# Performance work log

Measured on AMD Instinct MI355X. Metric: run time of the kernel, lower is better.

## Reference

```python
import jax, jax.numpy as jnp
import numpy as np

BN_EPS = 1e-5

# Binary activation with hardtanh STE semantics (forward: sign)
@jax.custom_vjp
def binary_act(x):
    return jnp.sign(x)

def _ba_fwd(x):
    return jnp.sign(x), x

def _ba_bwd(x, g):
    return (jnp.where(jnp.abs(x) > 1.0, 0.0, g),)

binary_act.defvjp(_ba_fwd, _ba_bwd)

# Binary weight quantizer (forward: sign, backward: identity STE)
@jax.custom_vjp
def binary_w(x):
    return jnp.sign(x)

def _bw_fwd(x):
    return jnp.sign(x), None

def _bw_bwd(_, g):
    return (g,)

binary_w.defvjp(_bw_fwd, _bw_bwd)


def setup_inputs() -> dict:
    key = jax.random.key(0)
    k1, k2, k3 = jax.random.split(key, 3)
    B, C_in, H, W_sp = 32, 256, 56, 56
    C_out, KH, KW = 256, 3, 3
    x = jax.random.normal(k1, (B, C_in, H, W_sp), dtype=jnp.float32)
    weight = jax.random.normal(k2, (C_out, C_in, KH, KW), dtype=jnp.float32) * 0.05
    bias = jax.random.normal(k3, (C_out,), dtype=jnp.float32) * 0.01
    gamma = jnp.ones((C_out,), dtype=jnp.float32)
    beta = jnp.zeros((C_out,), dtype=jnp.float32)
    return {"x": x, "weight": weight, "bias": bias, "gamma": gamma, "beta": beta}


def reference(x, weight, bias, gamma, beta):
    # --- activation binarization (A=2): sign ---
    xb = binary_act(x)
    # --- weight binarization (W=2): mean-center over in-channel dim, clamp, sign * alpha ---
    wc = weight - jnp.mean(weight, axis=1, keepdims=True)
    wc = jnp.clip(wc, -1.0, 1.0)
    alpha = jnp.mean(jnp.abs(wc), axis=(1, 2, 3), keepdims=True)  # per-output-channel scale
    wq = binary_w(wc) * alpha
    # --- conv2d, stride 1, padding 1 ---
    y = jax.lax.conv_general_dilated(
        xb, wq, window_strides=(1, 1), padding=((1, 1), (1, 1)),
        dimension_numbers=("NCHW", "OIHW", "NCHW"))
    y = y + bias[None, :, None, None]
    # --- BatchNorm2d (training-mode batch statistics, biased variance) ---
    mu = jnp.mean(y, axis=(0, 2, 3), keepdims=True)
    var = jnp.var(y, axis=(0, 2, 3), keepdims=True)
    y = (y - mu) * jax.lax.rsqrt(var + BN_EPS)
    y = y * gamma[None, :, None, None] + beta[None, :, None, None]
    # --- last_relu=1 ---
    y = jax.nn.relu(y)
    # --- last_bin=1 (A=2 -> binary activation) ---
    y = binary_act(y)
    return y
```

## Files before the change

### kernel.cpp

```cpp
#include <hip/hip_runtime.h>

typedef unsigned long long u64;
typedef int i32x4 __attribute__((ext_vector_type(4)));
typedef int i32x16 __attribute__((ext_vector_type(16)));

#define N_SP 3136
#define C_IN 256
#define C_OUT 256
#define BATCH 32
#define XROW 64
#define XPLANE (58 * XROW * 256)
#define XSIZE ((size_t)BATCH * XPLANE)

__global__ __launch_bounds__(256) void prep_weights(const float* __restrict__ w,
                                                    char* __restrict__ A_pack,
                                                    double* __restrict__ alpha,
                                                    u64* __restrict__ stats) {
    const int o = blockIdx.x;
    const int i = threadIdx.x;
    const int lane = i & 63, wvid = i >> 6;
    if (o == 0) { stats[i] = 0ull; stats[256 + i] = 0ull; }
    __shared__ double part[4][9];
    __shared__ double part2[4];

    float wv[9];
    const float* wp = w + ((size_t)o * C_IN + i) * 9;
#pragma unroll
    for (int t = 0; t < 9; ++t) wv[t] = wp[t];

#pragma unroll
    for (int t = 0; t < 9; ++t) {
        double v = (double)wv[t];
#pragma unroll
        for (int off = 32; off > 0; off >>= 1) v += __shfl_down(v, off);
        if (lane == 0) part[wvid][t] = v;
    }
    __syncthreads();

    double asum = 0.0;
#pragma unroll
    for (int t = 0; t < 9; ++t) {
        double mean = (part[0][t] + part[1][t] + part[2][t] + part[3][t]) * (1.0 / 256.0);
        double wc = (double)wv[t] - mean;
        int idx16 = ((t * 8 + (i >> 5)) * 8 + (o >> 5)) * 64 + (((i >> 4) & 1) << 5) + (o & 31);
        A_pack[(size_t)idx16 * 16 + (i & 15)] = (char)(wc > 0.0 ? 1 : -1);
        double aw = fabs(wc);
        if (aw > 1.0) aw = 1.0;
        asum += aw;
    }
#pragma unroll
    for (int off = 32; off > 0; off >>= 1) asum += __shfl_down(asum, off);
    if (lane == 0) part2[wvid] = asum;
    __syncthreads();
    if (i == 0)
        alpha[o] = (part2[0] + part2[1] + part2[2] + part2[3]) * (1.0 / 2304.0);
}

__global__ __launch_bounds__(256) void zero_borders(char* __restrict__ xsT) {
    const int tid = blockIdx.x * 256 + threadIdx.x;
    const int b = tid / 9216;
    const int r = tid - b * 9216;
    int hp, wp, c16;
    if (r < 2048) {
        hp = (r >> 10) * 57;
        wp = (r >> 4) & 63;
        c16 = (r & 15) << 4;
    } else {
        int r2 = r - 2048;
        hp = 1 + (r2 >> 7);
        int q = r2 & 127;
        int wi = q >> 4;
        wp = (wi == 0) ? 0 : 56 + wi;
        c16 = (q & 15) << 4;
    }
    *(i32x4*)(xsT + (((size_t)(b * 58 + hp) << 6) + wp) * 256 + c16) = (i32x4){0, 0, 0, 0};
}

__global__ __launch_bounds__(256) void sign_transpose(const float* __restrict__ x,
                                                      char* __restrict__ xsT) {
    const int sp0 = blockIdx.x * 64;
    const int b = blockIdx.y;
    const int lane = threadIdx.x & 63;
    const int wv = threadIdx.x >> 6;
    __shared__ char tile[64 * 272];

    const float* xp = x + ((size_t)(b * 256 + (wv << 6))) * N_SP + sp0 + lane;
#pragma unroll
    for (int q = 0; q < 4; ++q) {
        unsigned d[4];
#pragma unroll
        for (int dd = 0; dd < 4; ++dd) {
            unsigned v = 0;
#pragma unroll
            for (int kk = 0; kk < 4; ++kk) {
                int ci_l = (q << 4) + (dd << 2) + kk;
                float xv = xp[(size_t)ci_l * N_SP];
                v |= (unsigned)(xv > 0.0f ? 0x01u : 0xFFu) << (8 * kk);
            }
            d[dd] = v;
        }
        *(i32x4*)(tile + lane * 272 + (wv << 6) + (q << 4)) =
            (i32x4){(int)d[0], (int)d[1], (int)d[2], (int)d[3]};
    }
    __syncthreads();

    const int t = threadIdx.x;
#pragma unroll
    for (int j = 0; j < 4; ++j) {
        int sp_loc = (j << 4) + (t >> 4);
        int ci0 = (t & 15) << 4;
        i32x4 v = *(const i32x4*)(tile + sp_loc * 272 + ci0);
        int spg = sp0 + sp_loc;
        int h = spg / 56, w = spg - h * 56;
        size_t dst = (((size_t)(b * 58 + h + 1) << 6) + (w + 1)) * 256 + ci0;
        *(i32x4*)(xsT + dst) = v;
    }
}

__global__ __launch_bounds__(256, 2) void conv_mfma(const char* __restrict__ xsT,
                                                    const char* __restrict__ A_pack,
                                                    float* __restrict__ out) {
    const int tid = threadIdx.x;
    const int lane = tid & 63;
    const int wv = tid >> 6;
    const int l31 = lane & 31, l5 = lane >> 5;
    const int blk = blockIdx.x;
    const int b = blk / 28;
    const int h0 = (blk - b * 28) * 2;

    __shared__ char slab[4 * 66 * 272];

    {
        const char* src = xsT + ((size_t)(b * 58 + h0) << 6) * 256;
        for (int c = tid; c < 4 * 64 * 16; c += 256) {
            int dh = c >> 10, rem = c & 1023, wp = rem >> 4, c16 = (rem & 15) << 4;
            *(i32x4*)(slab + (dh * 66 + wp) * 272 + c16) =
                *(const i32x4*)(src + (size_t)dh * (XROW * 256) + wp * 256 + c16);
        }
        for (int c = tid; c < 128; c += 256) {
            int dh = c >> 5, wp = 64 + ((c >> 4) & 1), c16 = (c & 15) << 4;
            *(i32x4*)(slab + (dh * 66 + wp) * 272 + c16) = (i32x4){0, 0, 0, 0};
        }
    }
    __syncthreads();

    i32x16 acc[2][2][2] = {};

#pragma unroll
    for (int tap = 0; tap < 9; ++tap) {
        const int dh = tap / 3, dw = tap % 3;
#pragma unroll
        for (int cib = 0; cib < 8; ++cib) {
            i32x4 af[2];
#pragma unroll
            for (int a = 0; a < 2; ++a)
                af[a] = *(const i32x4*)(A_pack +
                    ((size_t)(((tap * 8 + cib) * 8 + wv * 2 + a) * 64 + lane) << 4));
            i32x4 bf[2][2];
#pragma unroll
            for (int nh = 0; nh < 2; ++nh)
#pragma unroll
                for (int row = 0; row < 2; ++row)
                    bf[nh][row] = *(const i32x4*)(slab +
                        ((dh + row) * 66 + (nh * 32 + l31) + dw) * 272 + l5 * 16 + cib * 32);
#pragma unroll
            for (int a = 0; a < 2; ++a)
#pragma unroll
                for (int nh = 0; nh < 2; ++nh)
#pragma unroll
                    for (int row = 0; row < 2; ++row)
                        acc[a][nh][row] = __builtin_amdgcn_mfma_i32_32x32x32_i8(
                            af[a], bf[nh][row], acc[a][nh][row], 0, 0, 0);
        }
    }

    float* ob = out + ((size_t)(b * 256 + wv * 64)) * N_SP + h0 * 56;
#pragma unroll
    for (int a = 0; a < 2; ++a)
#pragma unroll
        for (int nh = 0; nh < 2; ++nh) {
            const int w = nh * 32 + l31;
            if (w < 56) {
#pragma unroll
                for (int row = 0; row < 2; ++row)
#pragma unroll
                    for (int reg = 0; reg < 16; ++reg) {
                        int corow = (reg & 3) + 8 * (reg >> 2) + 4 * l5;
                        ob[(size_t)(a * 32 + corow) * N_SP + row * 56 + w] =
                            (float)acc[a][nh][row][reg];
                    }
            }
        }
}

__global__ __launch_bounds__(256) void stats_reduce(const float* __restrict__ out,
                                                    u64* __restrict__ stats) {
    const int c = blockIdx.x;
    const int sl = blockIdx.y;
    const int t = threadIdx.x;
    long long s1 = 0;
    u64 s2 = 0;
    for (int i = t; i < 4 * 784; i += 256) {
        int bl = i / 784, q = i - bl * 784;
        int b = sl * 4 + bl;
        float4 v = ((const float4*)out)[(size_t)(b * 256 + c) * 784 + q];
        int x0 = (int)v.x, x1 = (int)v.y, x2 = (int)v.z, x3 = (int)v.w;
        s1 += x0 + x1 + x2 + x3;
        s2 += (u64)((long long)x0 * x0 + (long long)x1 * x1 +
                    (long long)x2 * x2 + (long long)x3 * x3);
    }
#pragma unroll
    for (int off = 32; off > 0; off >>= 1) {
        s1 += __shfl_down(s1, off);
        s2 += __shfl_down(s2, off);
    }
    __shared__ long long p1[4];
    __shared__ u64 p2[4];
    if ((t & 63) == 0) { p1[t >> 6] = s1; p2[t >> 6] = s2; }
    __syncthreads();
    if (t == 0) {
        atomicAdd(&stats[c], (u64)(p1[0] + p1[1] + p1[2] + p1[3]));
        atomicAdd(&stats[C_OUT + c], p2[0] + p2[1] + p2[2] + p2[3]);
    }
}

__global__ void make_consts(const u64* __restrict__ stats,
                            const double* __restrict__ alpha,
                            const float* __restrict__ gamma,
                            const float* __restrict__ beta,
                            double* __restrict__ AB) {
    const int c = threadIdx.x;
    const double N = (double)(BATCH * N_SP);
    double s1 = (double)(long long)stats[c];
    double s2 = (double)(long long)stats[C_OUT + c];
    double mu = s1 / N;
    double var = s2 / N - mu * mu;
    double a = alpha[c];
    double vy = a * a * var;
    double scale = (double)gamma[c] / sqrt(vy + 1e-5);
    double A = a * scale;
    double B = (double)beta[c] - A * mu;
    AB[c] = A;
    AB[C_OUT + c] = B;
}

__global__ __launch_bounds__(256) void finalize(float* __restrict__ out,
                                                const double* __restrict__ AB) {
    const unsigned i4 = blockIdx.x * 256 + threadIdx.x;
    const unsigned e = i4 << 2;
    const int c = (int)((e / N_SP) & (C_OUT - 1));
    const double A = AB[c];
    const double B = AB[C_OUT + c];
    float4 v = ((float4*)out)[i4];
    v.x = (A * (double)v.x + B) > 0.0 ? 1.0f : 0.0f;
    v.y = (A * (double)v.y + B) > 0.0 ? 1.0f : 0.0f;
    v.z = (A * (double)v.z + B) > 0.0 ? 1.0f : 0.0f;
    v.w = (A * (double)v.w + B) > 0.0 ? 1.0f : 0.0f;
    ((float4*)out)[i4] = v;
}

extern "C" void kernel_launch(void* const* d_in, const int* in_sizes, int n_in,
                              void* d_out, int out_size, void* d_ws, size_t ws_size,
                              hipStream_t stream) {
    const float* x      = (const float*)d_in[0];
    const float* weight = (const float*)d_in[1];
    const float* bias   = (const float*)d_in[2];   (void)bias;
    const float* gamma  = (const float*)d_in[3];
    const float* beta   = (const float*)d_in[4];
    float* out = (float*)d_out;

    char* ws = (char*)d_ws;
    u64*    stats = (u64*)(ws);
    double* alpha = (double*)(ws + 4096);
    double* AB    = (double*)(ws + 8192);
    char*   A_pack = (char*)(ws + 16384);
    char*   xsT   = (char*)(ws + (1 << 20));

    prep_weights<<<C_OUT, 256, 0, stream>>>(weight, A_pack, alpha, stats);
    zero_borders<<<1152, 256, 0, stream>>>(xsT);
    sign_transpose<<<dim3(49, BATCH), 256, 0, stream>>>(x, xsT);
    conv_mfma<<<BATCH * 28, 256, 0, stream>>>(xsT, A_pack, out);
    stats_reduce<<<dim3(C_OUT, 8), 256, 0, stream>>>(out, stats);
    make_consts<<<1, C_OUT, 0, stream>>>(stats, alpha, gamma, beta, AB);
    finalize<<<(out_size / 4) / 256, 256, 0, stream>>>(out, AB);
}
```

Baseline: 357.4 us.

## Fuse BN statistics into conv epilogue and widen conv blocks to 8 waves

The conv kernel now computes per-channel sums and sums of squares from its accumulators and writes one partial per block and channel. A single small kernel reduces those partials and computes the BN constants, replacing the separate full re-read of the conv output, the atomics and the extra consts launch. Conv blocks go from 4 waves that each cover 64 output channels to 8 waves that each cover 32, which cuts accumulator registers per wave and raises wave count per block. Sums of squares are kept in 32-bit per block, which relies on the per-block values staying small enough not to overflow.

```diff
diff --git a/kernel.cpp b/kernel.cpp
--- a/kernel.cpp
+++ b/kernel.cpp
@@ -8,18 +8,17 @@
 #define C_IN 256
 #define C_OUT 256
 #define BATCH 32
+#define NBLK 896
 #define XROW 64
 #define XPLANE (58 * XROW * 256)
 #define XSIZE ((size_t)BATCH * XPLANE)
 
 __global__ __launch_bounds__(256) void prep_weights(const float* __restrict__ w,
                                                     char* __restrict__ A_pack,
-                                                    double* __restrict__ alpha,
-                                                    u64* __restrict__ stats) {
+                                                    double* __restrict__ alpha) {
     const int o = blockIdx.x;
     const int i = threadIdx.x;
     const int lane = i & 63, wvid = i >> 6;
-    if (o == 0) { stats[i] = 0ull; stats[256 + i] = 0ull; }
     __shared__ double part[4][9];
     __shared__ double part2[4];
 
@@ -117,9 +116,10 @@
     }
 }
 
-__global__ __launch_bounds__(256, 2) void conv_mfma(const char* __restrict__ xsT,
-                                                    const char* __restrict__ A_pack,
-                                                    float* __restrict__ out) {
+__global__ __launch_bounds__(512) void conv_mfma(const char* __restrict__ xsT,
+                                                 const char* __restrict__ A_pack,
+                                                 float* __restrict__ out,
+                                                 int2* __restrict__ partials) {
     const int tid = threadIdx.x;
     const int lane = tid & 63;
     const int wv = tid >> 6;
@@ -132,30 +132,27 @@
 
     {
         const char* src = xsT + ((size_t)(b * 58 + h0) << 6) * 256;
-        for (int c = tid; c < 4 * 64 * 16; c += 256) {
+        for (int c = tid; c < 4 * 64 * 16; c += 512) {
             int dh = c >> 10, rem = c & 1023, wp = rem >> 4, c16 = (rem & 15) << 4;
             *(i32x4*)(slab + (dh * 66 + wp) * 272 + c16) =
                 *(const i32x4*)(src + (size_t)dh * (XROW * 256) + wp * 256 + c16);
         }
-        for (int c = tid; c < 128; c += 256) {
-            int dh = c >> 5, wp = 64 + ((c >> 4) & 1), c16 = (c & 15) << 4;
+        if (tid < 128) {
+            int dh = tid >> 5, wp = 64 + ((tid >> 4) & 1), c16 = (tid & 15) << 4;
             *(i32x4*)(slab + (dh * 66 + wp) * 272 + c16) = (i32x4){0, 0, 0, 0};
         }
     }
     __syncthreads();
 
-    i32x16 acc[2][2][2] = {};
+    i32x16 acc[2][2] = {};
 
 #pragma unroll
     for (int tap = 0; tap < 9; ++tap) {
         const int dh = tap / 3, dw = tap % 3;
 #pragma unroll
         for (int cib = 0; cib < 8; ++cib) {
-            i32x4 af[2];
-#pragma unroll
-            for (int a = 0; a < 2; ++a)
-                af[a] = *(const i32x4*)(A_pack +
-                    ((size_t)(((tap * 8 + cib) * 8 + wv * 2 + a) * 64 + lane) << 4));
+            i32x4 af = *(const i32x4*)(A_pack +
+                ((size_t)(((tap * 8 + cib) * 8 + wv) * 64 + lane) << 4));
             i32x4 bf[2][2];
 #pragma unroll
             for (int nh = 0; nh < 2; ++nh)
@@ -164,84 +161,91 @@
                     bf[nh][row] = *(const i32x4*)(slab +
                         ((dh + row) * 66 + (nh * 32 + l31) + dw) * 272 + l5 * 16 + cib * 32);
 #pragma unroll
-            for (int a = 0; a < 2; ++a)
-#pragma unroll
-                for (int nh = 0; nh < 2; ++nh)
-#pragma unroll
-                    for (int row = 0; row < 2; ++row)
-                        acc[a][nh][row] = __builtin_amdgcn_mfma_i32_32x32x32_i8(
-                            af[a], bf[nh][row], acc[a][nh][row], 0, 0, 0);
-        }
-    }
-
-    float* ob = out + ((size_t)(b * 256 + wv * 64)) * N_SP + h0 * 56;
-#pragma unroll
-    for (int a = 0; a < 2; ++a)
-#pragma unroll
-        for (int nh = 0; nh < 2; ++nh) {
-            const int w = nh * 32 + l31;
-            if (w < 56) {
+            for (int nh = 0; nh < 2; ++nh)
 #pragma unroll
                 for (int row = 0; row < 2; ++row)
-#pragma unroll
-                    for (int reg = 0; reg < 16; ++reg) {
-                        int corow = (reg & 3) + 8 * (reg >> 2) + 4 * l5;
-                        ob[(size_t)(a * 32 + corow) * N_SP + row * 56 + w] =
-                            (float)acc[a][nh][row][reg];
-                    }
-            }
-        }
-}
-
-__global__ __launch_bounds__(256) void stats_reduce(const float* __restrict__ out,
-                                                    u64* __restrict__ stats) {
+                    acc[nh][row] = __builtin_amdgcn_mfma_i32_32x32x32_i8(
+                        af, bf[nh][row], acc[nh][row], 0, 0, 0);
+        }
+    }
+
+    float* ob = out + ((size_t)(b * 256 + wv * 32)) * N_SP + h0 * 56;
+#pragma unroll
+    for (int nh = 0; nh < 2; ++nh) {
+        const int w = nh * 32 + l31;
+        if (w < 56) {
+#pragma unroll
+            for (int row = 0; row < 2; ++row)
+#pragma unroll
+                for (int reg = 0; reg < 16; ++reg) {
+                    int corow = (reg & 3) + 8 * (reg >> 2) + 4 * l5;
+                    ob[(size_t)corow * N_SP + row * 56 + w] = (float)acc[nh][row][reg];
+                }
+        }
+    }
+
+    __syncthreads();
+    int* sp_s = (int*)slab;
+    int* sp_q = (int*)slab + 256;
+#pragma unroll
+    for (int reg = 0; reg < 16; ++reg) {
+        int v00 = acc[0][0][reg], v01 = acc[0][1][reg];
+        int v10 = (l31 < 24) ? acc[1][0][reg] : 0;
+        int v11 = (l31 < 24) ? acc[1][1][reg] : 0;
+        int s = v00 + v01 + v10 + v11;
+        unsigned q = (unsigned)(v00 * v00) + (unsigned)(v01 * v01)
+                   + (unsigned)(v10 * v10) + (unsigned)(v11 * v11);
+#pragma unroll
+        for (int off = 16; off > 0; off >>= 1) {
+            s += __shfl_xor(s, off);
+            q += (unsigned)__shfl_xor((int)q, off);
+        }
+        if (l31 == 0) {
+            int corow = (reg & 3) + 8 * (reg >> 2) + 4 * l5;
+            sp_s[wv * 32 + corow] = s;
+            sp_q[wv * 32 + corow] = (int)q;
+        }
+    }
+    __syncthreads();
+    if (tid < 256)
+        partials[(size_t)tid * NBLK + blk] = make_int2(sp_s[tid], sp_q[tid]);
+}
+
+__global__ __launch_bounds__(256) void stats_consts(const int2* __restrict__ partials,
+                                                    const double* __restrict__ alpha,
+                                                    const float* __restrict__ gamma,
+                                                    const float* __restrict__ beta,
+                                                    double* __restrict__ AB) {
     const int c = blockIdx.x;
-    const int sl = blockIdx.y;
     const int t = threadIdx.x;
-    long long s1 = 0;
-    u64 s2 = 0;
-    for (int i = t; i < 4 * 784; i += 256) {
-        int bl = i / 784, q = i - bl * 784;
-        int b = sl * 4 + bl;
-        float4 v = ((const float4*)out)[(size_t)(b * 256 + c) * 784 + q];
-        int x0 = (int)v.x, x1 = (int)v.y, x2 = (int)v.z, x3 = (int)v.w;
-        s1 += x0 + x1 + x2 + x3;
-        s2 += (u64)((long long)x0 * x0 + (long long)x1 * x1 +
-                    (long long)x2 * x2 + (long long)x3 * x3);
+    long long s1 = 0, s2 = 0;
+    for (int blk = t; blk < NBLK; blk += 256) {
+        int2 v = partials[(size_t)c * NBLK + blk];
+        s1 += v.x;
+        s2 += (long long)v.y;
     }
 #pragma unroll
     for (int off = 32; off > 0; off >>= 1) {
         s1 += __shfl_down(s1, off);
         s2 += __shfl_down(s2, off);
     }
-    __shared__ long long p1[4];
-    __shared__ u64 p2[4];
+    __shared__ long long p1[4], p2[4];
     if ((t & 63) == 0) { p1[t >> 6] = s1; p2[t >> 6] = s2; }
     __syncthreads();
     if (t == 0) {
-        atomicAdd(&stats[c], (u64)(p1[0] + p1[1] + p1[2] + p1[3]));
-        atomicAdd(&stats[C_OUT + c], p2[0] + p2[1] + p2[2] + p2[3]);
-    }
-}
-
-__global__ void make_consts(const u64* __restrict__ stats,
-                            const double* __restrict__ alpha,
-                            const float* __restrict__ gamma,
-                            const float* __restrict__ beta,
-                            double* __restrict__ AB) {
-    const int c = threadIdx.x;
-    const double N = (double)(BATCH * N_SP);
-    double s1 = (double)(long long)stats[c];
-    double s2 = (double)(long long)stats[C_OUT + c];
-    double mu = s1 / N;
-    double var = s2 / N - mu * mu;
-    double a = alpha[c];
-    double vy = a * a * var;
-    double scale = (double)gamma[c] / sqrt(vy + 1e-5);
-    double A = a * scale;
-    double B = (double)beta[c] - A * mu;
-    AB[c] = A;
-    AB[C_OUT + c] = B;
+        double S1 = (double)(p1[0] + p1[1] + p1[2] + p1[3]);
+        double S2 = (double)(p2[0] + p2[1] + p2[2] + p2[3]);
+        const double N = (double)(BATCH * N_SP);
+        double mu = S1 / N;
+        double var = S2 / N - mu * mu;
+        double a = alpha[c];
+        double vy = a * a * var;
+        double scale = (double)gamma[c] / sqrt(vy + 1e-5);
+        double A = a * scale;
+        double B = (double)beta[c] - A * mu;
+        AB[c] = A;
+        AB[C_OUT + c] = B;
+    }
 }
 
 __global__ __launch_bounds__(256) void finalize(float* __restrict__ out,
@@ -270,17 +274,16 @@
     float* out = (float*)d_out;
 
     char* ws = (char*)d_ws;
-    u64*    stats = (u64*)(ws);
     double* alpha = (double*)(ws + 4096);
     double* AB    = (double*)(ws + 8192);
     char*   A_pack = (char*)(ws + 16384);
     char*   xsT   = (char*)(ws + (1 << 20));
-
-    prep_weights<<<C_OUT, 256, 0, stream>>>(weight, A_pack, alpha, stats);
+    int2*   partials = (int2*)(ws + (1 << 20) + 31 * (1 << 20));
+
+    prep_weights<<<C_OUT, 256, 0, stream>>>(weight, A_pack, alpha);
     zero_borders<<<1152, 256, 0, stream>>>(xsT);
     sign_transpose<<<dim3(49, BATCH), 256, 0, stream>>>(x, xsT);
-    conv_mfma<<<BATCH * 28, 256, 0, stream>>>(xsT, A_pack, out);
-    stats_reduce<<<dim3(C_OUT, 8), 256, 0, stream>>>(out, stats);
-    make_consts<<<1, C_OUT, 0, stream>>>(stats, alpha, gamma, beta, AB);
+    conv_mfma<<<NBLK, 512, 0, stream>>>(xsT, A_pack, out, partials);
+    stats_consts<<<C_OUT, 256, 0, stream>>>(partials, alpha, gamma, beta, AB);
     finalize<<<(out_size / 4) / 256, 256, 0, stream>>>(out, AB);
 }
```

Result: slower. 378.9 us (+6.0%).
